# Optimization experiments

Hardware: AMD Instinct MI355X
Metric: run time of the kernel (lower is better)

## Reference

```python
import jax, jax.numpy as jnp
import numpy as np

B, S, D = 8, 2048, 768
N_SPANS = 512
MAX_W = 30  # static max span width (inclusive width in tokens)
H = 100
NEG = -1e30


def setup_inputs() -> dict:
    key = jax.random.key(0)
    k1, k2, k3, k4, k5, k6 = jax.random.split(key, 6)
    seq_tensor = jax.random.normal(k1, (B, S, D), dtype=jnp.float32)
    starts = jax.random.randint(k2, (B, N_SPANS), 0, S - MAX_W)
    widths = jax.random.randint(k3, (B, N_SPANS), 1, MAX_W + 1)  # span length in [1, MAX_W]
    ends_excl = starts + widths  # exclusive end, as module expects
    span_indices = jnp.stack([starts, ends_excl], axis=-1).astype(jnp.int64)
    span_mask = (jax.random.uniform(k4, (B, N_SPANS)) > 0.1).astype(jnp.int32)
    att_w = jax.random.normal(k5, (D, 1), dtype=jnp.float32) / np.sqrt(D)
    att_b = jnp.zeros((1,), dtype=jnp.float32)
    ffnn_w = jax.random.normal(k6, (D, H), dtype=jnp.float32) / np.sqrt(D)
    ffnn_b = jnp.zeros((H,), dtype=jnp.float32)
    return {"seq_tensor": seq_tensor, "span_indices": span_indices, "span_mask": span_mask,
            "att_w": att_w, "att_b": att_b, "ffnn_w": ffnn_w, "ffnn_b": ffnn_b}


def reference(seq_tensor, span_indices, span_mask, att_w, att_b, ffnn_w, ffnn_b):
    # exclusive end -> inclusive end (span_end_is_exclusive=True)
    starts = span_indices[..., 0]
    ends = span_indices[..., 1] - 1
    widths = ends - starts  # inclusive width - 1, in [0, MAX_W-1]

    offsets = jnp.arange(MAX_W)  # [W]
    raw_idx = starts[..., None] + offsets  # [B, N, W]
    width_mask = offsets <= widths[..., None]  # [B, N, W]
    idx = jnp.where(width_mask, raw_idx, 0)

    # global attention logits over the sequence: [B, S]
    att_logits = (jnp.einsum('bsd,do->bso', seq_tensor, att_w) + att_b)[..., 0]

    # gather span token embeddings and logits: [B, N, W, D], [B, N, W]
    span_emb = jax.vmap(lambda seq, i: seq[i])(seq_tensor, idx)
    span_logits = jax.vmap(lambda lg, i: lg[i])(att_logits, idx)

    # masked softmax over span width
    span_logits = jnp.where(width_mask, span_logits, NEG)
    attn = jax.nn.softmax(span_logits, axis=-1)  # [B, N, W]

    attended = jnp.einsum('bnw,bnwd->bnd', attn, span_emb)  # [B, N, D]
    attended = attended * span_mask.astype(attended.dtype)[..., None]

    # FeedForward: 1 layer Linear + tanh (dropout=0)
    out = jnp.tanh(jnp.einsum('bnd,dh->bnh', attended, ffnn_w) + ffnn_b)
    return out
```

## Files before the change

### kernel.cpp

```cpp
#include <hip/hip_runtime.h>
#include <cstdint>
#include <cstddef>

#define NB 8
#define NS 2048
#define ND 768
#define NSP 512
#define MAXW 30
#define NH 100
#define LDP 104
#define NKS 24
#define NCF 8
#define BM 32
#define BKF 64
#define NIT 12

typedef __attribute__((ext_vector_type(8))) short short8;
typedef __attribute__((ext_vector_type(4))) float floatx4;

union U4S8 { uint4 v; short8 s8; unsigned u[4]; unsigned short us[8]; };

__device__ inline unsigned short f2bf(float f) {
    unsigned u = __float_as_uint(f);
    return (unsigned short)((u + 0x7fffu + ((u >> 16) & 1u)) >> 16);
}

__device__ inline void split2(float x0, float x1, unsigned& hi, unsigned& lo) {
    unsigned u0 = __float_as_uint(x0), u1 = __float_as_uint(x1);
    unsigned h0 = u0 & 0xFFFF0000u, h1 = u1 & 0xFFFF0000u;
    hi = (u0 >> 16) | h1;
    float r0 = x0 - __uint_as_float(h0);
    float r1 = x1 - __uint_as_float(h1);
    lo = (__float_as_uint(r0) >> 16) | (__float_as_uint(r1) & 0xFFFF0000u);
}

__global__ __launch_bounds__(256) void pack_b_kernel(
    const float* __restrict__ ffnn_w, const float* __restrict__ att_w,
    uint4* __restrict__ Bfrag)
{
    int ks = blockIdx.x;
    for (int idx = threadIdx.x; idx < NCF * 64; idx += 256) {
        int cf = idx >> 6, lane = idx & 63;
        int q = lane >> 4, r = lane & 15;
        int n = cf * 16 + r;
        U4S8 p;
#pragma unroll
        for (int j = 0; j < 8; j++) {
            int k = ks * 32 + q * 8 + j;
            float v = (n < NH) ? ffnn_w[(size_t)k * NH + n]
                               : (n == NH ? att_w[k] : 0.f);
            p.us[j] = f2bf(v);
        }
        Bfrag[(size_t)(ks * NCF + cf) * 64 + lane] = p.v;
    }
}

__global__ __launch_bounds__(256) void proj_kernel(
    const float* __restrict__ seq, const uint4* __restrict__ Bfrag,
    float* __restrict__ P, float* __restrict__ Lg)
{
    __shared__ float As[BM][BKF + 4];
    const int t = threadIdx.x;
    const int wave = t >> 6, lane = t & 63;
    const int q = lane >> 4, r = lane & 15;
    const int wr = wave & 1, wc = wave >> 1;
    const int cf0 = wc * 4;
    const int row0 = blockIdx.x * BM;

    floatx4 acc[4] = {{0.f,0.f,0.f,0.f},{0.f,0.f,0.f,0.f},
                      {0.f,0.f,0.f,0.f},{0.f,0.f,0.f,0.f}};

    const int sr = t >> 4, sc = t & 15;
    const float4* gA0 = (const float4*)(seq + (size_t)(row0 + sr) * ND);
    const float4* gA1 = (const float4*)(seq + (size_t)(row0 + 16 + sr) * ND);
    float* w0 = &As[sr][sc * 4];
    float* w1 = &As[16 + sr][sc * 4];

    float4 s0 = gA0[sc], s1 = gA1[sc];

    const float* rdbase = &As[wr * 16 + r][q * 8];
    const uint4* bp = Bfrag + (size_t)cf0 * 64 + lane;

    for (int i = 0; i < NIT; ++i) {
        __syncthreads();
        *(float4*)w0 = s0;
        *(float4*)w1 = s1;
        __syncthreads();
        const int nx = (i + 1 < NIT ? i + 1 : i) * 16 + sc;
        s0 = gA0[nx]; s1 = gA1[nx];

        uint4 Bv[8];
#pragma unroll
        for (int ksl = 0; ksl < 2; ++ksl)
#pragma unroll
            for (int c = 0; c < 4; ++c)
                Bv[ksl * 4 + c] = bp[(size_t)((i * 2 + ksl) * NCF) * 64 + c * 64];

#pragma unroll
        for (int ksl = 0; ksl < 2; ++ksl) {
            float4 a0 = *(const float4*)(rdbase + ksl * 32);
            float4 a1 = *(const float4*)(rdbase + ksl * 32 + 4);
            U4S8 hi, lo;
            split2(a0.x, a0.y, hi.u[0], lo.u[0]);
            split2(a0.z, a0.w, hi.u[1], lo.u[1]);
            split2(a1.x, a1.y, hi.u[2], lo.u[2]);
            split2(a1.z, a1.w, hi.u[3], lo.u[3]);
#pragma unroll
            for (int c = 0; c < 4; ++c) {
                U4S8 b; b.v = Bv[ksl * 4 + c];
                acc[c] = __builtin_amdgcn_mfma_f32_16x16x32_bf16(hi.s8, b.s8, acc[c], 0, 0, 0);
                acc[c] = __builtin_amdgcn_mfma_f32_16x16x32_bf16(lo.s8, b.s8, acc[c], 0, 0, 0);
            }
        }
    }

#pragma unroll
    for (int c = 0; c < 4; ++c) {
        const int col = (cf0 + c) * 16 + r;
        const int rowb = row0 + wr * 16 + q * 4;
        if (col < NH) {
#pragma unroll
            for (int reg = 0; reg < 4; ++reg)
                P[(size_t)(rowb + reg) * LDP + col] = acc[c][reg];
        } else if (col == NH) {
#pragma unroll
            for (int reg = 0; reg < 4; ++reg)
                Lg[rowb + reg] = acc[c][reg];
        }
    }
}

__global__ __launch_bounds__(256) void span_kernel(
    const int* __restrict__ span_idx, const int* __restrict__ span_mask,
    const float* __restrict__ P, const float* __restrict__ Lg,
    const float* __restrict__ ffnn_b, float* __restrict__ out)
{
    const int wave = threadIdx.x >> 6, lane = threadIdx.x & 63;
    const int gs = blockIdx.x * 4 + wave;
    const int b = gs / NSP;
    const int st = span_idx[2 * gs];
    int w = span_idx[2 * gs + 1] - st;
    w = max(1, min(w, MAXW));

    float lg = -1e30f;
    if (lane < w) lg = Lg[b * NS + st + lane];
    float mx = lg;
#pragma unroll
    for (int off = 32; off > 0; off >>= 1) mx = fmaxf(mx, __shfl_xor(mx, off));
    float e = (lane < w) ? __expf(lg - mx) : 0.f;
    float sum = e;
#pragma unroll
    for (int off = 32; off > 0; off >>= 1) sum += __shfl_xor(sum, off);
    float attn = e / sum;

    int cl = min(lane, 24);
    const float4* Pb4 = (const float4*)(P + ((size_t)b * NS + st) * LDP) + cl;
    float4 acc = {0.f, 0.f, 0.f, 0.f};
#pragma unroll
    for (int i = 0; i < MAXW; ++i) {
        float a = __shfl(attn, i);
        float4 v = Pb4[i * (LDP / 4)];
        acc.x += a * v.x; acc.y += a * v.y; acc.z += a * v.z; acc.w += a * v.w;
    }

    if (lane < 25) {
        float m = (float)span_mask[gs];
        float4 bias = ((const float4*)ffnn_b)[lane];
        float4 o;
        o.x = tanhf(m * acc.x + bias.x);
        o.y = tanhf(m * acc.y + bias.y);
        o.z = tanhf(m * acc.z + bias.z);
        o.w = tanhf(m * acc.w + bias.w);
        *(float4*)(out + (size_t)gs * NH + 4 * lane) = o;
    }
}

extern "C" void kernel_launch(void* const* d_in, const int* in_sizes, int n_in,
                              void* d_out, int out_size, void* d_ws, size_t ws_size,
                              hipStream_t stream) {
    const float* seq      = (const float*)d_in[0];
    const int*   span_idx = (const int*)d_in[1];
    const int*   span_msk = (const int*)d_in[2];
    const float* att_w    = (const float*)d_in[3];
    const float* ffnn_w   = (const float*)d_in[5];
    const float* ffnn_b   = (const float*)d_in[6];
    float* out = (float*)d_out;

    char* ws = (char*)d_ws;
    size_t off = 0;
    float* P     = (float*)(ws + off); off += (size_t)NB * NS * LDP * 4;
    uint4* Bfrag = (uint4*)(ws + off); off += (size_t)NKS * NCF * 64 * 16;
    float* Lg    = (float*)(ws + off);

    pack_b_kernel<<<NKS, 256, 0, stream>>>(ffnn_w, att_w, Bfrag);
    proj_kernel<<<(NB * NS) / BM, 256, 0, stream>>>(seq, Bfrag, P, Lg);
    span_kernel<<<(NB * NSP) / 4, 256, 0, stream>>>(span_idx, span_msk, P, Lg, ffnn_b, out);
}
```

Baseline: 118.5 us.

## Shrink projection tile, pre-split A into bf16 hi/lo, and use half-wave span work

The projection kernel now uses 16-row tiles, so it launches twice as many blocks. Each wave owns two column fragments instead of four. Each thread splits its float4 into bf16 hi/lo once before storing to separate LDS arrays, rather than every reader splitting after the LDS read, and B fragments are prefetched one iteration ahead in registers. The span kernel now assigns one span per 32-lane half-wave, giving 8 spans per block, and skips loads past the span width. These changes aim to raise occupancy and cut redundant split and memory traffic, at the cost of less B-fragment reuse per block and more divergent branches.

```diff
diff --git a/kernel.cpp b/kernel.cpp
--- a/kernel.cpp
+++ b/kernel.cpp
@@ -11,8 +11,7 @@
 #define LDP 104
 #define NKS 24
 #define NCF 8
-#define BM 32
-#define BKF 64
+#define BM 16
 #define NIT 12
 
 typedef __attribute__((ext_vector_type(8))) short short8;
@@ -55,69 +54,60 @@
     }
 }
 
-__global__ __launch_bounds__(256) void proj_kernel(
+__global__ __launch_bounds__(256, 4) void proj_kernel(
     const float* __restrict__ seq, const uint4* __restrict__ Bfrag,
     float* __restrict__ P, float* __restrict__ Lg)
 {
-    __shared__ float As[BM][BKF + 4];
+    __shared__ unsigned Ahi[BM][36];
+    __shared__ unsigned Alo[BM][36];
     const int t = threadIdx.x;
     const int wave = t >> 6, lane = t & 63;
     const int q = lane >> 4, r = lane & 15;
-    const int wr = wave & 1, wc = wave >> 1;
-    const int cf0 = wc * 4;
+    const int cf0 = wave * 2;
     const int row0 = blockIdx.x * BM;
 
-    floatx4 acc[4] = {{0.f,0.f,0.f,0.f},{0.f,0.f,0.f,0.f},
-                      {0.f,0.f,0.f,0.f},{0.f,0.f,0.f,0.f}};
+    floatx4 acc[2] = {{0.f,0.f,0.f,0.f},{0.f,0.f,0.f,0.f}};
 
     const int sr = t >> 4, sc = t & 15;
-    const float4* gA0 = (const float4*)(seq + (size_t)(row0 + sr) * ND);
-    const float4* gA1 = (const float4*)(seq + (size_t)(row0 + 16 + sr) * ND);
-    float* w0 = &As[sr][sc * 4];
-    float* w1 = &As[16 + sr][sc * 4];
+    const float4* gA = (const float4*)(seq + (size_t)(row0 + sr) * ND);
+    float4 sv = gA[sc];
 
-    float4 s0 = gA0[sc], s1 = gA1[sc];
-
-    const float* rdbase = &As[wr * 16 + r][q * 8];
     const uint4* bp = Bfrag + (size_t)cf0 * 64 + lane;
+    uint4 Bc0 = bp[0], Bc1 = bp[64], Bc2 = bp[512], Bc3 = bp[512 + 64];
 
     for (int i = 0; i < NIT; ++i) {
+        unsigned h01, l01, h23, l23;
+        split2(sv.x, sv.y, h01, l01);
+        split2(sv.z, sv.w, h23, l23);
         __syncthreads();
-        *(float4*)w0 = s0;
-        *(float4*)w1 = s1;
+        { uint2 u; u.x = h01; u.y = h23; *(uint2*)&Ahi[sr][sc * 2] = u; }
+        { uint2 u; u.x = l01; u.y = l23; *(uint2*)&Alo[sr][sc * 2] = u; }
         __syncthreads();
-        const int nx = (i + 1 < NIT ? i + 1 : i) * 16 + sc;
-        s0 = gA0[nx]; s1 = gA1[nx];
 
-        uint4 Bv[8];
-#pragma unroll
-        for (int ksl = 0; ksl < 2; ++ksl)
-#pragma unroll
-            for (int c = 0; c < 4; ++c)
-                Bv[ksl * 4 + c] = bp[(size_t)((i * 2 + ksl) * NCF) * 64 + c * 64];
+        const int ni = (i + 1 < NIT) ? i + 1 : i;
+        sv = gA[ni * 16 + sc];
+        const size_t nb = (size_t)ni * 1024;
+        uint4 Bn0 = bp[nb], Bn1 = bp[nb + 64], Bn2 = bp[nb + 512], Bn3 = bp[nb + 512 + 64];
 
 #pragma unroll
         for (int ksl = 0; ksl < 2; ++ksl) {
-            float4 a0 = *(const float4*)(rdbase + ksl * 32);
-            float4 a1 = *(const float4*)(rdbase + ksl * 32 + 4);
-            U4S8 hi, lo;
-            split2(a0.x, a0.y, hi.u[0], lo.u[0]);
-            split2(a0.z, a0.w, hi.u[1], lo.u[1]);
-            split2(a1.x, a1.y, hi.u[2], lo.u[2]);
-            split2(a1.z, a1.w, hi.u[3], lo.u[3]);
-#pragma unroll
-            for (int c = 0; c < 4; ++c) {
-                U4S8 b; b.v = Bv[ksl * 4 + c];
-                acc[c] = __builtin_amdgcn_mfma_f32_16x16x32_bf16(hi.s8, b.s8, acc[c], 0, 0, 0);
-                acc[c] = __builtin_amdgcn_mfma_f32_16x16x32_bf16(lo.s8, b.s8, acc[c], 0, 0, 0);
-            }
+            U4S8 ah, al, b0, b1;
+            ah.v = *(const uint4*)&Ahi[r][ksl * 16 + q * 4];
+            al.v = *(const uint4*)&Alo[r][ksl * 16 + q * 4];
+            b0.v = ksl ? Bc2 : Bc0;
+            b1.v = ksl ? Bc3 : Bc1;
+            acc[0] = __builtin_amdgcn_mfma_f32_16x16x32_bf16(ah.s8, b0.s8, acc[0], 0, 0, 0);
+            acc[0] = __builtin_amdgcn_mfma_f32_16x16x32_bf16(al.s8, b0.s8, acc[0], 0, 0, 0);
+            acc[1] = __builtin_amdgcn_mfma_f32_16x16x32_bf16(ah.s8, b1.s8, acc[1], 0, 0, 0);
+            acc[1] = __builtin_amdgcn_mfma_f32_16x16x32_bf16(al.s8, b1.s8, acc[1], 0, 0, 0);
         }
+        Bc0 = Bn0; Bc1 = Bn1; Bc2 = Bn2; Bc3 = Bn3;
     }
 
 #pragma unroll
-    for (int c = 0; c < 4; ++c) {
+    for (int c = 0; c < 2; ++c) {
         const int col = (cf0 + c) * 16 + r;
-        const int rowb = row0 + wr * 16 + q * 4;
+        const int rowb = row0 + q * 4;
         if (col < NH) {
 #pragma unroll
             for (int reg = 0; reg < 4; ++reg)
@@ -130,27 +120,26 @@
     }
 }
 
-__global__ __launch_bounds__(256) void span_kernel(
+__global__ __launch_bounds__(256, 4) void span_kernel(
     const int* __restrict__ span_idx, const int* __restrict__ span_mask,
     const float* __restrict__ P, const float* __restrict__ Lg,
     const float* __restrict__ ffnn_b, float* __restrict__ out)
 {
-    const int wave = threadIdx.x >> 6, lane = threadIdx.x & 63;
-    const int gs = blockIdx.x * 4 + wave;
+    const int hw = threadIdx.x >> 5, lane = threadIdx.x & 31;
+    const int gs = blockIdx.x * 8 + hw;
     const int b = gs / NSP;
     const int st = span_idx[2 * gs];
     int w = span_idx[2 * gs + 1] - st;
     w = max(1, min(w, MAXW));
 
-    float lg = -1e30f;
-    if (lane < w) lg = Lg[b * NS + st + lane];
+    float lg = (lane < w) ? Lg[b * NS + st + lane] : -1e30f;
     float mx = lg;
 #pragma unroll
-    for (int off = 32; off > 0; off >>= 1) mx = fmaxf(mx, __shfl_xor(mx, off));
+    for (int off = 16; off > 0; off >>= 1) mx = fmaxf(mx, __shfl_xor(mx, off, 32));
     float e = (lane < w) ? __expf(lg - mx) : 0.f;
     float sum = e;
 #pragma unroll
-    for (int off = 32; off > 0; off >>= 1) sum += __shfl_xor(sum, off);
+    for (int off = 16; off > 0; off >>= 1) sum += __shfl_xor(sum, off, 32);
     float attn = e / sum;
 
     int cl = min(lane, 24);
@@ -158,9 +147,11 @@
     float4 acc = {0.f, 0.f, 0.f, 0.f};
 #pragma unroll
     for (int i = 0; i < MAXW; ++i) {
-        float a = __shfl(attn, i);
-        float4 v = Pb4[i * (LDP / 4)];
-        acc.x += a * v.x; acc.y += a * v.y; acc.z += a * v.z; acc.w += a * v.w;
+        float a = __shfl(attn, i, 32);
+        if (i < w) {
+            float4 v = Pb4[i * (LDP / 4)];
+            acc.x += a * v.x; acc.y += a * v.y; acc.z += a * v.z; acc.w += a * v.w;
+        }
     }
 
     if (lane < 25) {
@@ -194,5 +185,5 @@
 
     pack_b_kernel<<<NKS, 256, 0, stream>>>(ffnn_w, att_w, Bfrag);
     proj_kernel<<<(NB * NS) / BM, 256, 0, stream>>>(seq, Bfrag, P, Lg);
-    span_kernel<<<(NB * NSP) / 4, 256, 0, stream>>>(span_idx, span_msk, P, Lg, ffnn_b, out);
+    span_kernel<<<(NB * NSP) / 8, 256, 0, stream>>>(span_idx, span_msk, P, Lg, ffnn_b, out);
 }
```

Result: faster. 115.5 us (-2.5%).
